# Kernel tuning notes

Measured on AMD Instinct MI355X. Metric: run time of the kernel, lower is better.

## Reference

```python
import jax, jax.numpy as jnp
import numpy as np

N = 65536      # total nodes
B = 512        # graphs (equal-sized)
NPER = N // B  # 128 nodes per graph
E = 655360     # edges
F_IN = 128
K = 32         # sort-pool k
OUT = 27


def _gcn(x, row, col, dinv, W, b):
    # PyG GCNConv with added self-loops and symmetric normalization:
    xw = x @ W                                   # [N, F_out]
    coef = dinv[row] * dinv[col]                 # [E]
    agg = jax.ops.segment_sum(xw[row] * coef[:, None], col, num_segments=N)
    return agg + (dinv * dinv)[:, None] * xw + b  # self-loop term + bias


def _conv1d(x, w, b, stride):
    # x: [B, C_in, L], w: [C_out, C_in, K]
    out = jax.lax.conv_general_dilated(x, w, (stride,), 'VALID',
                                       dimension_numbers=('NCH', 'OIH', 'NCH'))
    return out + b[None, :, None]


def setup_inputs() -> dict:
    key = jax.random.key(0)
    ks = jax.random.split(key, 16)
    x = jax.random.normal(ks[0], (N, F_IN), dtype=jnp.float32)
    edge_index = jax.random.randint(ks[1], (2, E), 0, N, dtype=jnp.int32)
    batch = jnp.repeat(jnp.arange(B, dtype=jnp.int32), NPER)

    def lin(k, fi, fo):
        return jax.random.normal(k, (fi, fo), dtype=jnp.float32) / np.sqrt(fi)

    W1, b1 = lin(ks[2], F_IN, 128), jnp.zeros((128,), jnp.float32)
    W2, b2 = lin(ks[3], 128, 64), jnp.zeros((64,), jnp.float32)
    W3, b3 = lin(ks[4], 64, 32), jnp.zeros((32,), jnp.float32)
    W4, b4 = lin(ks[5], 32, 32), jnp.zeros((32,), jnp.float32)
    conv5_w = jax.random.normal(ks[6], (16, 1, 256), jnp.float32) / np.sqrt(256)
    conv5_b = jnp.zeros((16,), jnp.float32)
    conv6_w = jax.random.normal(ks[7], (32, 16, 5), jnp.float32) / np.sqrt(16 * 5)
    conv6_b = jnp.zeros((32,), jnp.float32)
    dense_w = lin(ks[8], 384, OUT)
    dense_b = jnp.zeros((OUT,), jnp.float32)
    return dict(x=x, edge_index=edge_index, batch=batch,
                W1=W1, b1=b1, W2=W2, b2=b2, W3=W3, b3=b3, W4=W4, b4=b4,
                conv5_w=conv5_w, conv5_b=conv5_b, conv6_w=conv6_w, conv6_b=conv6_b,
                dense_w=dense_w, dense_b=dense_b)


def reference(x, edge_index, batch, W1, b1, W2, b2, W3, b3, W4, b4,
              conv5_w, conv5_b, conv6_w, conv6_b, dense_w, dense_b):
    row, col = edge_index[0], edge_index[1]
    deg = jax.ops.segment_sum(jnp.ones((E,), x.dtype), col, num_segments=N) + 1.0
    dinv = jax.lax.rsqrt(deg)

    x1 = jnp.tanh(_gcn(x, row, col, dinv, W1, b1))
    x2 = jnp.tanh(_gcn(x1, row, col, dinv, W2, b2))
    x3 = jnp.tanh(_gcn(x2, row, col, dinv, W3, b3))
    x4 = jnp.tanh(_gcn(x3, row, col, dinv, W4, b4))
    h = jnp.concatenate([x1, x2, x3, x4], axis=-1)   # [N, 256]

    # SortAggregation: sort nodes within each graph by last channel (desc), take top-k.
    hg = h.reshape(B, NPER, 256)
    idx = jnp.argsort(-hg[:, :, -1], axis=1)[:, :K]                 # [B, K]
    pooled = jnp.take_along_axis(hg, idx[:, :, None], axis=1)       # [B, K, 256]
    top_k_indices = idx + (jnp.arange(B, dtype=idx.dtype) * NPER)[:, None]

    z = pooled.reshape(B, 1, K * 256)                # [B, 1, 8192]
    z = jax.nn.relu(_conv1d(z, conv5_w, conv5_b, 256))  # [B, 16, 32]
    z = jax.lax.reduce_window(z, -jnp.inf, jax.lax.max,
                              (1, 1, 2), (1, 1, 2), 'VALID')        # [B, 16, 16]
    z = jax.nn.relu(_conv1d(z, conv6_w, conv6_b, 1))  # [B, 32, 12]
    z = z.reshape(B, -1)                              # [B, 384]
    out = z @ dense_w + dense_b                       # [B, 27]
    return out, top_k_indices
```

## Files before the change

kernel.cpp:

```cpp
#include <hip/hip_runtime.h>
#include <math.h>

#define N_NODES 65536
#define N_EDGES 655360
#define N_GRAPHS 512
#define NPERG 128
#define KTOP 32
#define NOUT 27
#define OUT0_SIZE (N_GRAPHS * NOUT)
#define EPS 64

typedef unsigned int uint32;
typedef unsigned short u16;
typedef unsigned char u8;
typedef __attribute__((ext_vector_type(8))) short bf16x8;
typedef __attribute__((ext_vector_type(4))) float f32x4;
typedef __attribute__((ext_vector_type(2))) float f32x2;
typedef __attribute__((ext_vector_type(4))) float f32x4n;

__device__ __forceinline__ float blo(uint32 u) { return __uint_as_float(u << 16); }
__device__ __forceinline__ float bhi(uint32 u) { return __uint_as_float(u & 0xffff0000u); }
__device__ __forceinline__ u16 f2b(float f) {
    uint32 u = __float_as_uint(f);
    u += 0x7fffu + ((u >> 16) & 1u);
    return (u16)(u >> 16);
}
__device__ __forceinline__ uint32 pk(float a, float b) {
    return (uint32)f2b(a) | ((uint32)f2b(b) << 16);
}
__device__ __forceinline__ f32x2 fp8lo(uint32 u) { return __builtin_amdgcn_cvt_pk_f32_fp8((int)u, false); }
__device__ __forceinline__ f32x2 fp8hi(uint32 u) { return __builtin_amdgcn_cvt_pk_f32_fp8((int)u, true); }
__device__ __forceinline__ u8 f2fp8(float v) {
    return (u8)(__builtin_amdgcn_cvt_pk_fp8_f32(v, v, 0, false) & 0xff);
}
__device__ __forceinline__ float ftanh(float x) {
    float t = __builtin_amdgcn_exp2f(x * 2.8853900817779268f);
    return 1.0f - 2.0f * __builtin_amdgcn_rcpf(t + 1.0f);
}


template<int FI, int FO>
__device__ __forceinline__ void pack_w(const float* __restrict__ W, uint4* __restrict__ pw,
                                       int base, int nb) {
    constexpr int KC = FI / 8;
    for (int q = (blockIdx.x - base) * 256 + threadIdx.x; q < FO * KC; q += nb * 256) {
        int n = q % FO, c = q / FO;
        const float* wp = W + (size_t)(c * 8) * FO + n;
        uint4 v;
        v.x = pk(wp[0],            wp[(size_t)FO]);
        v.y = pk(wp[2*(size_t)FO], wp[3*(size_t)FO]);
        v.z = pk(wp[4*(size_t)FO], wp[5*(size_t)FO]);
        v.w = pk(wp[6*(size_t)FO], wp[7*(size_t)FO]);
        pw[n * KC + c] = v;
    }
}

__global__ __launch_bounds__(256) void prep_kernel(const float* __restrict__ W1, const float* __restrict__ W2,
                                                   const float* __restrict__ W3, const float* __restrict__ W4,
                                                   uint4* __restrict__ pw1, uint4* __restrict__ pw2,
                                                   uint4* __restrict__ pw3, uint4* __restrict__ pw4,
                                                   int* __restrict__ cur) {
    int b = blockIdx.x;
    if (b < 256) { cur[b * 256 + threadIdx.x] = 0; return; }
    b -= 256;
    if (b < 8)       pack_w<128, 128>(W1, pw1, 256, 8);
    else if (b < 12) pack_w<128, 64>(W2, pw2, 264, 4);
    else if (b < 13) pack_w<64, 32>(W3, pw3, 268, 1);
    else             pack_w<32, 32>(W4, pw4, 269, 1);
}


__global__ __launch_bounds__(256) void fill_kernel(const int* __restrict__ erow, const int* __restrict__ ecol,
                                                   int* __restrict__ cur, u16* __restrict__ ep) {
    int e = blockIdx.x * 256 + threadIdx.x;
    int r = __builtin_nontemporal_load(erow + e);
    int d = __builtin_nontemporal_load(ecol + e);
    int slot = atomicAdd(&cur[d], 1);
    if (slot < EPS) ep[(d << 6) + slot] = (u16)r;
}


template<int FI, int FO>
__device__ __forceinline__ void stage_Bp(const uint4* __restrict__ pw, uint4* __restrict__ Bs) {
    constexpr int KC = FI / 8, SA = KC + 1;
    for (int q = threadIdx.x; q < FO * KC; q += 256) {
        int n = q / KC, c = q % KC;
        Bs[n * SA + c] = pw[q];
    }
}

template<int FI, int FO, bool OUT_FP8>
__device__ __forceinline__ void mfma_store(uint4* __restrict__ As, const uint4* __restrict__ Bs,
                                           uint4* __restrict__ Y, size_t rowbase,
                                           const float* __restrict__ ds) {
    constexpr int KC = FI / 8, SA = KC + 1;
    constexpr int NTILE = FO / 16;
    constexpr int CW = (NTILE >= 4) ? 4 : NTILE;
    constexpr int NTW = NTILE / CW;
    constexpr int RW = 4 / CW;
    constexpr int RS = 2 / RW;
    constexpr int KSTEPS = FI / 32;
    int t = threadIdx.x;
    int w = t >> 6, L = t & 63;
    int quad = L >> 4, m = L & 15;
    int cw = w % CW, rw = w / CW;

    const bf16x8* Asv = (const bf16x8*)As;
    const bf16x8* Bsv = (const bf16x8*)Bs;

    f32x4 acc[RS][NTW];
#pragma unroll
    for (int i = 0; i < RS; i++)
#pragma unroll
        for (int j = 0; j < NTW; j++) acc[i][j] = (f32x4)0.f;

#pragma unroll
    for (int ks = 0; ks < KSTEPS; ks++) {
        int kc = ks * 4 + quad;
        bf16x8 bfr[NTW];
#pragma unroll
        for (int j = 0; j < NTW; j++) {
            int n = (cw * NTW + j) * 16 + m;
            bfr[j] = Bsv[n * SA + kc];
        }
#pragma unroll
        for (int i = 0; i < RS; i++) {
            int r = (rw * RS + i) * 16 + m;
            bf16x8 afr = Asv[r * SA + kc];
#pragma unroll
            for (int j = 0; j < NTW; j++)
                acc[i][j] = __builtin_amdgcn_mfma_f32_16x16x32_bf16(afr, bfr[j], acc[i][j], 0, 0, 0);
        }
    }
    __syncthreads();

    if constexpr (OUT_FP8) {
        u8* outs = (u8*)As;
#pragma unroll
        for (int i = 0; i < RS; i++) {
            int rb = (rw * RS + i) * 16 + quad * 4;
#pragma unroll
            for (int j = 0; j < NTW; j++) {
                int cc = (cw * NTW + j) * 16 + m;
#pragma unroll
                for (int g2 = 0; g2 < 4; g2++)
                    outs[(rb + g2) * FO + cc] = f2fp8(acc[i][j][g2] * ds[rb + g2]);
            }
        }
    } else {
        u16* outs = (u16*)As;
#pragma unroll
        for (int i = 0; i < RS; i++) {
            int rb = (rw * RS + i) * 16 + quad * 4;
#pragma unroll
            for (int j = 0; j < NTW; j++) {
                int cc = (cw * NTW + j) * 16 + m;
#pragma unroll
                for (int g2 = 0; g2 < 4; g2++)
                    outs[(rb + g2) * FO + cc] = f2b(acc[i][j][g2] * ds[rb + g2]);
            }
        }
    }
    __syncthreads();
    constexpr int NU4 = OUT_FP8 ? (32 * FO / 16) : (32 * FO / 8);
    for (int q = t; q < NU4; q += 256)
        Y[rowbase * (NU4 / 32) + q] = ((const uint4*)As)[q];
}


__global__ __launch_bounds__(256) void gemm1_kernel(const float* __restrict__ x,
                                                    const uint4* __restrict__ pw1,
                                                    const int* __restrict__ cur,
                                                    uint4* __restrict__ xw1) {
    constexpr int KC = 16, SA = 17;
    __shared__ __align__(16) uint4 As[32 * SA];
    __shared__ __align__(16) uint4 Bs[128 * SA];
    __shared__ float ds[32];
    int t = threadIdx.x;
    stage_Bp<128, 128>(pw1, Bs);
    size_t rowbase = (size_t)blockIdx.x * 32;
    if (t < 32) ds[t] = rsqrtf((float)cur[rowbase + t] + 1.0f);
    for (int q = t; q < 32 * KC; q += 256) {
        int r = q / KC, c = q % KC;
        const f32x4n* xp4 = (const f32x4n*)(x + (rowbase + r) * 128 + c * 8);
        f32x4n v0 = __builtin_nontemporal_load(xp4);
        f32x4n v1 = __builtin_nontemporal_load(xp4 + 1);
        uint4 u;
        u.x = pk(v0.x, v0.y); u.y = pk(v0.z, v0.w);
        u.z = pk(v1.x, v1.y); u.w = pk(v1.z, v1.w);
        As[r * SA + c] = u;
    }
    __syncthreads();
    mfma_store<128, 128, true>(As, Bs, xw1, rowbase, ds);
}


template<int F>
__device__ __forceinline__ void gath8_fp8v(const uint2* __restrict__ x2, uint4 e8,
                                           int cl, int rem, float (&ac)[8]) {
    constexpr int LN = F / 8;
    uint32 qq[8] = { e8.x & 0xffffu, e8.x >> 16, e8.y & 0xffffu, e8.y >> 16,
                     e8.z & 0xffffu, e8.z >> 16, e8.w & 0xffffu, e8.w >> 16 };
#pragma unroll
    for (int j = 0; j < 8; j++) {
        bool ok = j < rem;
        uint32 src = ok ? qq[j] : 0u;
        uint2 g = x2[(size_t)src * LN + cl];
        uint32 gx = ok ? g.x : 0u, gy = ok ? g.y : 0u;
        f32x2 l0 = fp8lo(gx), h0 = fp8hi(gx), l1 = fp8lo(gy), h1 = fp8hi(gy);
        ac[0] += l0.x; ac[1] += l0.y; ac[2] += h0.x; ac[3] += h0.y;
        ac[4] += l1.x; ac[5] += l1.y; ac[6] += h1.x; ac[7] += h1.y;
    }
}

template<int F>
__device__ __forceinline__ void agg_node_fp8v(const uint2* __restrict__ x2,
                                              const u16* __restrict__ ep,
                                              int n, int cl, int deg, float dn,
                                              const float* __restrict__ bias, float (&r)[8]) {
    constexpr int LN = F / 8;
    const u16* epp = ep + (n << 6);
    float ac[8];
#pragma unroll
    for (int c = 0; c < 8; c++) ac[c] = 0.f;
    uint4 e0 = *(const uint4*)(epp);
    uint4 e1 = *(const uint4*)(epp + 8);
    gath8_fp8v<F>(x2, e0, cl, deg, ac);
    gath8_fp8v<F>(x2, e1, cl, deg - 8, ac);
    if (deg > 16) {
        int nb = min((deg + 7) >> 3, EPS / 8);
        for (int b = 2; b < nb; b++) {
            uint4 e8 = *(const uint4*)(epp + b * 8);
            gath8_fp8v<F>(x2, e8, cl, deg - b * 8, ac);
        }
    }
    uint2 sv = x2[(size_t)n * LN + cl];
    f32x2 l0 = fp8lo(sv.x), h0 = fp8hi(sv.x), l1 = fp8lo(sv.y), h1 = fp8hi(sv.y);
    float sf[8] = { l0.x, l0.y, h0.x, h0.y, l1.x, l1.y, h1.x, h1.y };
#pragma unroll
    for (int c = 0; c < 8; c++) r[c] = dn * (ac[c] + sf[c]) + bias[8 * cl + c];
}


template<int F, int FO, bool OUT_FP8>
__global__ __launch_bounds__(256, 6) void agg_gemm8(const uint2* __restrict__ xin,
                                                    const int* __restrict__ cur,
                                                    const u16* __restrict__ ep,
                                                    const float* __restrict__ bias,
                                                    const uint4* __restrict__ pw,
                                                    uint4* __restrict__ hc4, int co4,
                                                    uint4* __restrict__ xout) {
    constexpr int KC = F / 8, SA = KC + 1;
    constexpr int LN = F / 8;
    constexpr int NPP = 256 / LN;
    __shared__ __align__(16) uint4 As[32 * SA];
    __shared__ __align__(16) uint4 Bs[FO * SA];
    __shared__ float ds[32];
    int t = threadIdx.x;
    int rowbase = blockIdx.x * 32;
    stage_Bp<F, FO>(pw, Bs);
    if (t < 32) ds[t] = rsqrtf((float)cur[rowbase + t] + 1.0f);
    __syncthreads();

    int cl = t % LN, nsub = t / LN;
#pragma unroll
    for (int pass = 0; pass < 32 / NPP; pass++) {
        int nl = pass * NPP + nsub;
        int n = rowbase + nl;
        int deg = cur[n];
        float r[8];
        agg_node_fp8v<F>(xin, ep, n, cl, deg, ds[nl], bias, r);
        uint4 pr;
        pr.x = pk(ftanh(r[0]), ftanh(r[1]));
        pr.y = pk(ftanh(r[2]), ftanh(r[3]));
        pr.z = pk(ftanh(r[4]), ftanh(r[5]));
        pr.w = pk(ftanh(r[6]), ftanh(r[7]));
        hc4[(size_t)n * 32 + co4 + cl] = pr;
        As[nl * SA + cl] = pr;
    }
    __syncthreads();
    mfma_store<F, FO, OUT_FP8>(As, Bs, xout, (size_t)rowbase, ds);
}


template<int L4>
__device__ __forceinline__ void gath8_bf16(const uint2* __restrict__ x2, uint4 e8,
                                           int c4, int rem, float (&ac)[4][4]) {
    uint32 qq[8] = { e8.x & 0xffffu, e8.x >> 16, e8.y & 0xffffu, e8.y >> 16,
                     e8.z & 0xffffu, e8.z >> 16, e8.w & 0xffffu, e8.w >> 16 };
#pragma unroll
    for (int j = 0; j < 8; j++) {
        bool ok = j < rem;
        uint32 src = ok ? qq[j] : 0u;
        uint2 g = x2[(size_t)src * L4 + c4];
        uint32 gx = ok ? g.x : 0u, gy = ok ? g.y : 0u;
        ac[j & 3][0] += blo(gx); ac[j & 3][1] += bhi(gx);
        ac[j & 3][2] += blo(gy); ac[j & 3][3] += bhi(gy);
    }
}

template<int F>
__device__ __forceinline__ void agg_node_bf16(const uint2* __restrict__ x2,
                                              const u16* __restrict__ ep,
                                              int n, int c4, int deg, float dn,
                                              const float* __restrict__ bias,
                                              float& r0, float& r1, float& r2, float& r3) {
    constexpr int L4 = F / 4;
    const u16* epp = ep + (n << 6);
    float ac[4][4];
#pragma unroll
    for (int i = 0; i < 4; i++)
#pragma unroll
        for (int j = 0; j < 4; j++) ac[i][j] = 0.f;
    uint4 e0 = *(const uint4*)(epp);
    uint4 e1 = *(const uint4*)(epp + 8);
    gath8_bf16<L4>(x2, e0, c4, deg, ac);
    gath8_bf16<L4>(x2, e1, c4, deg - 8, ac);
    if (deg > 16) {
        int nb = min((deg + 7) >> 3, EPS / 8);
        for (int b = 2; b < nb; b++) {
            uint4 e8 = *(const uint4*)(epp + b * 8);
            gath8_bf16<L4>(x2, e8, c4, deg - b * 8, ac);
        }
    }
    float s0 = (ac[0][0] + ac[1][0]) + (ac[2][0] + ac[3][0]);
    float s1 = (ac[0][1] + ac[1][1]) + (ac[2][1] + ac[3][1]);
    float s2 = (ac[0][2] + ac[1][2]) + (ac[2][2] + ac[3][2]);
    float s3 = (ac[0][3] + ac[1][3]) + (ac[2][3] + ac[3][3]);
    uint2 sv = x2[(size_t)n * L4 + c4];
    r0 = dn * (s0 + blo(sv.x)) + bias[4 * c4 + 0];
    r1 = dn * (s1 + bhi(sv.x)) + bias[4 * c4 + 1];
    r2 = dn * (s2 + blo(sv.y)) + bias[4 * c4 + 2];
    r3 = dn * (s3 + bhi(sv.y)) + bias[4 * c4 + 3];
}


template<int F, int FO>
__global__ __launch_bounds__(256, 6) void agg_gemm_bf(const uint32* __restrict__ xin,
                                                      const int* __restrict__ cur,
                                                      const u16* __restrict__ ep,
                                                      const float* __restrict__ bias,
                                                      const uint4* __restrict__ pw,
                                                      uint32* __restrict__ hc, int co2,
                                                      uint4* __restrict__ xout) {
    constexpr int KC = F / 8, SA = KC + 1;
    constexpr int L4 = F / 4;
    constexpr int NPP = 256 / L4;
    __shared__ __align__(16) uint4 As[32 * SA];
    __shared__ __align__(16) uint4 Bs[FO * SA];
    __shared__ float ds[32];
    int t = threadIdx.x;
    int rowbase = blockIdx.x * 32;
    stage_Bp<F, FO>(pw, Bs);
    if (t < 32) ds[t] = rsqrtf((float)cur[rowbase + t] + 1.0f);
    __syncthreads();

    uint2* As2 = (uint2*)As;
    uint2* hc2 = (uint2*)hc;
    int c4 = t % L4;
    int nsub = t / L4;
#pragma unroll
    for (int pass = 0; pass < 32 / NPP; pass++) {
        int nl = pass * NPP + nsub;
        int n = rowbase + nl;
        int deg = cur[n];
        float r0, r1, r2, r3;
        agg_node_bf16<F>((const uint2*)xin, ep, n, c4, deg, ds[nl], bias, r0, r1, r2, r3);
        uint2 pr;
        pr.x = pk(ftanh(r0), ftanh(r1));
        pr.y = pk(ftanh(r2), ftanh(r3));
        hc2[(size_t)n * 64 + co2 + c4] = pr;
        As2[nl * (SA * 2) + c4] = pr;
    }
    __syncthreads();
    mfma_store<F, FO, false>(As, Bs, xout, (size_t)rowbase, ds);
}


__device__ __forceinline__ void key_g8(const uint32* __restrict__ xw, uint4 e8,
                                       int rem, float (&ac3)[4]) {
    uint32 qq[8] = { e8.x & 0xffffu, e8.x >> 16, e8.y & 0xffffu, e8.y >> 16,
                     e8.z & 0xffffu, e8.z >> 16, e8.w & 0xffffu, e8.w >> 16 };
#pragma unroll
    for (int j = 0; j < 8; j++) {
        bool ok = j < rem;
        uint32 src = ok ? qq[j] : 0u;
        uint32 gy = xw[(size_t)src * 16 + 15];
        ac3[j & 3] += bhi(ok ? gy : 0u);
    }
}

__global__ __launch_bounds__(256) void final_kernel(const uint32* __restrict__ hc,
                                                    const uint32* __restrict__ xw4,
                                                    const int* __restrict__ cur,
                                                    const u16* __restrict__ ep,
                                                    const float* __restrict__ b4,
                                                    const float* __restrict__ w5, const float* __restrict__ b5,
                                                    const float* __restrict__ w6, const float* __restrict__ b6,
                                                    const float* __restrict__ dw, const float* __restrict__ db,
                                                    float* __restrict__ out) {
    __shared__ float skey[128];
    __shared__ int   sidx[KTOP];
    __shared__ uint32 ph[32 * 133];
    __shared__ __align__(16) float w5s[4096];
    __shared__ float z5[16 * 33];
    __shared__ float ms[16 * 17];
    __shared__ float z6[384];
    int g = blockIdx.x, t = threadIdx.x;

    if (t >= 128) {
        for (int q = t - 128; q < 1024; q += 128)
            ((float4*)w5s)[q] = ((const float4*)w5)[q];
    } else {
        int n = g * NPERG + t;
        int deg = cur[n];
        float dn = rsqrtf((float)deg + 1.0f);
        const u16* epp = ep + (n << 6);
        float ac3[4] = { 0.f, 0.f, 0.f, 0.f };
        uint4 e0 = *(const uint4*)(epp);
        uint4 e1 = *(const uint4*)(epp + 8);
        key_g8(xw4, e0, deg, ac3);
        key_g8(xw4, e1, deg - 8, ac3);
        if (deg > 16) {
            int nb = min((deg + 7) >> 3, EPS / 8);
            for (int b = 2; b < nb; b++) {
                uint4 e8 = *(const uint4*)(epp + b * 8);
                key_g8(xw4, e8, deg - b * 8, ac3);
            }
        }
        float s3 = (ac3[0] + ac3[1]) + (ac3[2] + ac3[3]);
        uint32 svy = xw4[(size_t)n * 16 + 15];
        float r3 = dn * (s3 + bhi(svy)) + b4[31];
        skey[t] = __uint_as_float(((uint32)f2b(ftanh(r3))) << 16);
    }
    __syncthreads();

    if (t < 128) {
        float ki = skey[t];
        int rank = 0;
#pragma unroll 16
        for (int j = 0; j < 128; j++) {
            float kj = skey[j];
            rank += (kj > ki) || (kj == ki && j < t);
        }
        if (rank < KTOP) {
            sidx[rank] = t;
            out[OUT0_SIZE + g * KTOP + rank] = (float)(g * NPERG + t);
        }
    }
    __syncthreads();

    {
        int r = t >> 3, c4 = t & 7;
        int n = g * NPERG + sidx[r];
        int deg = cur[n];
        float dn = rsqrtf((float)deg + 1.0f);
        float r0, r1, r2, r3;
        agg_node_bf16<32>((const uint2*)xw4, ep, n, c4, deg, dn, b4, r0, r1, r2, r3);
        uint32* dst = &ph[r * 133 + 112 + 2 * c4];
        dst[0] = pk(ftanh(r0), ftanh(r1));
        dst[1] = pk(ftanh(r2), ftanh(r3));
    }

    {
        const uint4* hcv = (const uint4*)hc;
        for (int q = t; q < 1024; q += 256) {
            int cell = q & 31;
            if (cell >= 28) continue;
            int r2 = q >> 5;
            int node = g * NPERG + sidx[r2];
            uint4 v = hcv[(size_t)node * 32 + cell];
            uint32* dst = &ph[r2 * 133 + cell * 4];
            dst[0] = v.x; dst[1] = v.y; dst[2] = v.z; dst[3] = v.w;
        }
    }
    __syncthreads();

    {
        int o = t >> 5, l = t & 31;
        float a0 = 0.f, a1 = 0.f;
#pragma unroll 4
        for (int j2 = 0; j2 < 128; j2++) {
            uint32 u = ph[l * 133 + j2];
            float p0 = blo(u), p1 = bhi(u);
            a0 += p0 * w5s[o * 256 + 2 * j2]       + p1 * w5s[o * 256 + 2 * j2 + 1];
            a1 += p0 * w5s[(o + 8) * 256 + 2 * j2] + p1 * w5s[(o + 8) * 256 + 2 * j2 + 1];
        }
        z5[o * 33 + l]       = fmaxf(a0 + b5[o], 0.f);
        z5[(o + 8) * 33 + l] = fmaxf(a1 + b5[o + 8], 0.f);
    }
    __syncthreads();

    {
        int o = t >> 4, p = t & 15;
        ms[o * 17 + p] = fmaxf(z5[o * 33 + 2 * p], z5[o * 33 + 2 * p + 1]);
    }
    __syncthreads();

    for (int q = t; q < 384; q += 256) {
        int o2 = q / 12, tt = q % 12;
        float a = b6[o2];
        for (int o = 0; o < 16; o++) {
#pragma unroll
            for (int k = 0; k < 5; k++)
                a += w6[(o2 * 16 + o) * 5 + k] * ms[o * 17 + tt + k];
        }
        z6[q] = fmaxf(a, 0.f);
    }
    __syncthreads();

    if (t < NOUT) {
        float a = db[t];
        for (int i = 0; i < 384; i++) a += z6[i] * dw[i * NOUT + t];
        out[g * NOUT + t] = a;
    }
}


extern "C" void kernel_launch(void* const* d_in, const int* in_sizes, int n_in,
                              void* d_out, int out_size, void* d_ws, size_t ws_size,
                              hipStream_t stream) {
    const float* x    = (const float*)d_in[0];
    const int*   edge = (const int*)d_in[1];
    const int*   erow = edge;
    const int*   ecol = edge + N_EDGES;
    const float* W1 = (const float*)d_in[3];  const float* b1 = (const float*)d_in[4];
    const float* W2 = (const float*)d_in[5];  const float* b2 = (const float*)d_in[6];
    const float* W3 = (const float*)d_in[7];  const float* b3 = (const float*)d_in[8];
    const float* W4 = (const float*)d_in[9];  const float* b4 = (const float*)d_in[10];
    const float* w5 = (const float*)d_in[11]; const float* b5 = (const float*)d_in[12];
    const float* w6 = (const float*)d_in[13]; const float* b6 = (const float*)d_in[14];
    const float* dw = (const float*)d_in[15]; const float* db = (const float*)d_in[16];
    float* out = (float*)d_out;

    char* wsb = (char*)d_ws;
    size_t off = 0;
    auto alloc = [&](size_t bytes) -> void* {
        void* p = wsb + off;
        off = (off + bytes + 255) & ~(size_t)255;
        return p;
    };
    int*    cur  = (int*)   alloc((size_t)N_NODES * 4);
    u16*    ep   = (u16*)   alloc((size_t)N_NODES * EPS * 2);
    uint32* xwA  = (uint32*)alloc((size_t)N_NODES * 32 * 4);
    uint32* xwB  = (uint32*)alloc((size_t)N_NODES * 32 * 4);
    uint32* hc   = (uint32*)alloc((size_t)N_NODES * 128 * 4);
    uint4*  pw1  = (uint4*) alloc(2048 * 16);
    uint4*  pw2  = (uint4*) alloc(1024 * 16);
    uint4*  pw3  = (uint4*) alloc(256 * 16);
    uint4*  pw4  = (uint4*) alloc(128 * 16);
    (void)ws_size; (void)in_sizes; (void)n_in; (void)out_size;

    prep_kernel<<<270, 256, 0, stream>>>(W1, W2, W3, W4, pw1, pw2, pw3, pw4, cur);
    fill_kernel<<<N_EDGES / 256, 256, 0, stream>>>(erow, ecol, cur, ep);
    gemm1_kernel<<<N_NODES / 32, 256, 0, stream>>>(x, pw1, cur, (uint4*)xwA);
    agg_gemm8<128, 64, true><<<N_NODES / 32, 256, 0, stream>>>((const uint2*)xwA, cur, ep, b1, pw2, (uint4*)hc, 0, (uint4*)xwB);
    agg_gemm8<64, 32, false><<<N_NODES / 32, 256, 0, stream>>>((const uint2*)xwB, cur, ep, b2, pw3, (uint4*)hc, 16, (uint4*)xwA);
    agg_gemm_bf<32, 32><<<N_NODES / 32, 256, 0, stream>>>(xwA, cur, ep, b3, pw4, hc, 48, (uint4*)xwB);
    final_kernel<<<N_GRAPHS, 256, 0, stream>>>(hc, xwB, cur, ep, b4, w5, b5, w6, b6, dw, db, out);
}
```

Baseline: 233.1 us.

## Loop gemm1 over multiple tiles per block, raise occupancy bounds, drop w5 LDS staging

gemm1 now processes three 32-row tiles per block on a smaller grid, so the 128x128 packed weight staging into LDS is amortised over several tiles. The 64->32 aggregation kernel and agg_gemm_bf get a higher launch_bounds minimum-waves hint (8 instead of 6) to push occupancy. The final kernel stops copying conv5 weights into LDS and reads them as float4 straight from global memory, which cuts LDS use and removes the copy. The risks are register spills under the tighter bounds and extra global traffic for the weight reads.

```diff
diff --git a/kernel.cpp b/kernel.cpp
--- a/kernel.cpp
+++ b/kernel.cpp
@@ -168,6 +168,9 @@
 }
 
 
+#define G1_TILES 3
+#define G1_GRID  683
+
 __global__ __launch_bounds__(256) void gemm1_kernel(const float* __restrict__ x,
                                                     const uint4* __restrict__ pw1,
                                                     const int* __restrict__ cur,
@@ -178,20 +181,26 @@
     __shared__ float ds[32];
     int t = threadIdx.x;
     stage_Bp<128, 128>(pw1, Bs);
-    size_t rowbase = (size_t)blockIdx.x * 32;
-    if (t < 32) ds[t] = rsqrtf((float)cur[rowbase + t] + 1.0f);
-    for (int q = t; q < 32 * KC; q += 256) {
-        int r = q / KC, c = q % KC;
-        const f32x4n* xp4 = (const f32x4n*)(x + (rowbase + r) * 128 + c * 8);
-        f32x4n v0 = __builtin_nontemporal_load(xp4);
-        f32x4n v1 = __builtin_nontemporal_load(xp4 + 1);
-        uint4 u;
-        u.x = pk(v0.x, v0.y); u.y = pk(v0.z, v0.w);
-        u.z = pk(v1.x, v1.y); u.w = pk(v1.z, v1.w);
-        As[r * SA + c] = u;
-    }
-    __syncthreads();
-    mfma_store<128, 128, true>(As, Bs, xw1, rowbase, ds);
+#pragma unroll 1
+    for (int tile = 0; tile < G1_TILES; tile++) {
+        int tb = blockIdx.x * G1_TILES + tile;
+        if (tb >= N_NODES / 32) break;
+        size_t rowbase = (size_t)tb * 32;
+        if (t < 32) ds[t] = rsqrtf((float)cur[rowbase + t] + 1.0f);
+        __syncthreads();
+        for (int q = t; q < 32 * KC; q += 256) {
+            int r = q / KC, c = q % KC;
+            const f32x4n* xp4 = (const f32x4n*)(x + (rowbase + r) * 128 + c * 8);
+            f32x4n v0 = __builtin_nontemporal_load(xp4);
+            f32x4n v1 = __builtin_nontemporal_load(xp4 + 1);
+            uint4 u;
+            u.x = pk(v0.x, v0.y); u.y = pk(v0.z, v0.w);
+            u.z = pk(v1.x, v1.y); u.w = pk(v1.z, v1.w);
+            As[r * SA + c] = u;
+        }
+        __syncthreads();
+        mfma_store<128, 128, true>(As, Bs, xw1, rowbase, ds);
+    }
 }
 
 
@@ -242,14 +251,14 @@
 }
 
 
-template<int F, int FO, bool OUT_FP8>
-__global__ __launch_bounds__(256, 6) void agg_gemm8(const uint2* __restrict__ xin,
-                                                    const int* __restrict__ cur,
-                                                    const u16* __restrict__ ep,
-                                                    const float* __restrict__ bias,
-                                                    const uint4* __restrict__ pw,
-                                                    uint4* __restrict__ hc4, int co4,
-                                                    uint4* __restrict__ xout) {
+template<int F, int FO, bool OUT_FP8, int WPE>
+__global__ __launch_bounds__(256, WPE) void agg_gemm8(const uint2* __restrict__ xin,
+                                                      const int* __restrict__ cur,
+                                                      const u16* __restrict__ ep,
+                                                      const float* __restrict__ bias,
+                                                      const uint4* __restrict__ pw,
+                                                      uint4* __restrict__ hc4, int co4,
+                                                      uint4* __restrict__ xout) {
     constexpr int KC = F / 8, SA = KC + 1;
     constexpr int LN = F / 8;
     constexpr int NPP = 256 / LN;
@@ -336,7 +345,7 @@
 
 
 template<int F, int FO>
-__global__ __launch_bounds__(256, 6) void agg_gemm_bf(const uint32* __restrict__ xin,
+__global__ __launch_bounds__(256, 8) void agg_gemm_bf(const uint32* __restrict__ xin,
                                                       const int* __restrict__ cur,
                                                       const u16* __restrict__ ep,
                                                       const float* __restrict__ bias,
@@ -402,16 +411,12 @@
     __shared__ float skey[128];
     __shared__ int   sidx[KTOP];
     __shared__ uint32 ph[32 * 133];
-    __shared__ __align__(16) float w5s[4096];
     __shared__ float z5[16 * 33];
     __shared__ float ms[16 * 17];
     __shared__ float z6[384];
     int g = blockIdx.x, t = threadIdx.x;
 
-    if (t >= 128) {
-        for (int q = t - 128; q < 1024; q += 128)
-            ((float4*)w5s)[q] = ((const float4*)w5)[q];
-    } else {
+    if (t < 128) {
         int n = g * NPERG + t;
         int deg = cur[n];
         float dn = rsqrtf((float)deg + 1.0f);
@@ -478,13 +483,20 @@
 
     {
         int o = t >> 5, l = t & 31;
+        const float4* w5a = (const float4*)(w5 + o * 256);
+        const float4* w5b = (const float4*)(w5 + (o + 8) * 256);
         float a0 = 0.f, a1 = 0.f;
 #pragma unroll 4
-        for (int j2 = 0; j2 < 128; j2++) {
-            uint32 u = ph[l * 133 + j2];
-            float p0 = blo(u), p1 = bhi(u);
-            a0 += p0 * w5s[o * 256 + 2 * j2]       + p1 * w5s[o * 256 + 2 * j2 + 1];
-            a1 += p0 * w5s[(o + 8) * 256 + 2 * j2] + p1 * w5s[(o + 8) * 256 + 2 * j2 + 1];
+        for (int j4 = 0; j4 < 64; j4++) {
+            float4 wa = w5a[j4];
+            float4 wb = w5b[j4];
+            uint32 u0 = ph[l * 133 + 2 * j4];
+            uint32 u1 = ph[l * 133 + 2 * j4 + 1];
+            float p0 = blo(u0), p1 = bhi(u0), p2 = blo(u1), p3 = bhi(u1);
+            a0 += p0 * wa.x + p1 * wa.y;
+            a0 += p2 * wa.z + p3 * wa.w;
+            a1 += p0 * wb.x + p1 * wb.y;
+            a1 += p2 * wb.z + p3 * wb.w;
         }
         z5[o * 33 + l]       = fmaxf(a0 + b5[o], 0.f);
         z5[(o + 8) * 33 + l] = fmaxf(a1 + b5[o + 8], 0.f);
@@ -553,9 +565,9 @@
 
     prep_kernel<<<270, 256, 0, stream>>>(W1, W2, W3, W4, pw1, pw2, pw3, pw4, cur);
     fill_kernel<<<N_EDGES / 256, 256, 0, stream>>>(erow, ecol, cur, ep);
-    gemm1_kernel<<<N_NODES / 32, 256, 0, stream>>>(x, pw1, cur, (uint4*)xwA);
-    agg_gemm8<128, 64, true><<<N_NODES / 32, 256, 0, stream>>>((const uint2*)xwA, cur, ep, b1, pw2, (uint4*)hc, 0, (uint4*)xwB);
-    agg_gemm8<64, 32, false><<<N_NODES / 32, 256, 0, stream>>>((const uint2*)xwB, cur, ep, b2, pw3, (uint4*)hc, 16, (uint4*)xwA);
+    gemm1_kernel<<<G1_GRID, 256, 0, stream>>>(x, pw1, cur, (uint4*)xwA);
+    agg_gemm8<128, 64, true, 6><<<N_NODES / 32, 256, 0, stream>>>((const uint2*)xwA, cur, ep, b1, pw2, (uint4*)hc, 0, (uint4*)xwB);
+    agg_gemm8<64, 32, false, 8><<<N_NODES / 32, 256, 0, stream>>>((const uint2*)xwB, cur, ep, b2, pw3, (uint4*)hc, 16, (uint4*)xwA);
     agg_gemm_bf<32, 32><<<N_NODES / 32, 256, 0, stream>>>(xwA, cur, ep, b3, pw4, hc, 48, (uint4*)xwB);
     final_kernel<<<N_GRAPHS, 256, 0, stream>>>(hc, xwB, cur, ep, b4, w5, b5, w6, b6, dw, db, out);
 }
```

Measured after the change: 238.0 us. 2.1% more time.
